# Kernel tuning notes

Measured on AMD Instinct MI355X. Metric: run time of the kernel, lower is better.

## Reference

```python
import jax, jax.numpy as jnp
import numpy as np

B, S, D = 1, 4096, 1024
H, Dh = 16, 64
F = 4096  # mlp_factor * D
EPS = 1e-6


def _ln(x, scale, bias=None):
    m = jnp.mean(x, axis=-1, keepdims=True)
    v = jnp.var(x, axis=-1, keepdims=True)
    y = (x - m) * jax.lax.rsqrt(v + EPS) * scale
    return y + bias if bias is not None else y


def setup_inputs() -> dict:
    key = jax.random.key(0)
    ks = jax.random.split(key, 10)
    lecun = lambda k, shape, fan_in: (jax.random.normal(k, shape, jnp.float32) * (fan_in ** -0.5))
    inp = {
        "x": jax.random.normal(ks[0], (B, S, D), jnp.float32),
        # causal mask, broadcastable to [B, H, S, S]
        "mask": jnp.tril(jnp.ones((S, S), bool))[None, None],
        # PreNorm (TPNorm -> LayerNorm)
        "ln_scale": jnp.ones((D,), jnp.float32),
        "ln_bias": jnp.zeros((D,), jnp.float32),
        # MLP input projection
        "w_in": lecun(ks[1], (D, F), D),
        "b_in": jnp.zeros((F,), jnp.float32),
        # QKV projection
        "wq": lecun(ks[2], (D, H, Dh), D),
        "bq": jnp.zeros((H, Dh), jnp.float32),
        "wk": lecun(ks[3], (D, H, Dh), D),
        "bk": jnp.zeros((H, Dh), jnp.float32),
        "wv": lecun(ks[4], (D, H, Dh), D),
        "bv": jnp.zeros((H, Dh), jnp.float32),
        # qk-norm scales (normalize_qk=True)
        "qn_scale": jnp.ones((Dh,), jnp.float32),
        "kn_scale": jnp.ones((Dh,), jnp.float32),
        # MLP output projection
        "w_mo": lecun(ks[5], (F, D), F),
        "b_mo": jnp.zeros((D,), jnp.float32),
        # Attention output projection
        "w_ao": lecun(ks[6], (H * Dh, D), H * Dh),
        "b_ao": jnp.zeros((D,), jnp.float32),
    }
    return inp


def reference(x, mask, ln_scale, ln_bias, w_in, b_in, wq, bq, wk, bk, wv, bv,
              qn_scale, kn_scale, w_mo, b_mo, w_ao, b_ao):
    residual = x
    xn = _ln(x, ln_scale, ln_bias)

    # fused QKV + MLP-input projections (QKVMLPDenseParallel)
    h = jax.nn.gelu(jnp.einsum("bsd,df->bsf", xn, w_in) + b_in)  # [B,S,F]
    q = jnp.einsum("bsd,dhk->bshk", xn, wq) + bq  # [B,S,H,Dh]
    k = jnp.einsum("bsd,dhk->bshk", xn, wk) + bk
    v = jnp.einsum("bsd,dhk->bshk", xn, wv) + bv
    # normalize_qk: per-head LayerNorm (no bias) on q, k
    q = _ln(q, qn_scale)
    k = _ln(k, kn_scale)

    # dot-product attention
    scores = jnp.einsum("bqhd,bkhd->bhqk", q, k) / np.sqrt(Dh).astype(np.float32)
    scores = jnp.where(mask, scores, jnp.finfo(scores.dtype).min)
    attn = jax.nn.softmax(scores, axis=-1)
    o = jnp.einsum("bhqk,bkhd->bqhd", attn, v)  # [B,S,H,Dh]

    # fused attention-out + MLP-out projections (AttnMLPOutParallel)
    mlp_out = jnp.einsum("bsf,fd->bsd", h, w_mo) + b_mo
    attn_out = jnp.einsum("bse,ed->bsd", o.reshape(B, S, H * Dh), w_ao) + b_ao

    # dropout deterministic (train=False); residual add
    return residual + mlp_out + attn_out
```

## Files before the change

kernel.cpp:

```cpp
#include <hip/hip_runtime.h>
#include <hip/hip_fp16.h>

typedef _Float16 half8 __attribute__((ext_vector_type(8)));
typedef float floatx4 __attribute__((ext_vector_type(4)));

constexpr int kS = 4096;
constexpr int kD = 1024;
constexpr int kH = 16;
constexpr int kDh = 64;
constexpr int kF = 4096;
constexpr int kNQKV = kF + 3 * kD;
constexpr int kKOut = kF + kD;

__device__ __forceinline__ void async_ld16(const void* g, void* l) {
  __builtin_amdgcn_global_load_lds(
      (const __attribute__((address_space(1))) void*)g,
      (__attribute__((address_space(3))) void*)l, 16, 0, 0);
}

__global__ __launch_bounds__(256) void prep0_kernel(
    const float* __restrict__ w_in, const float* __restrict__ wq,
    const float* __restrict__ wk, const float* __restrict__ wv,
    const float* __restrict__ w_mo, const float* __restrict__ w_ao,
    _Float16* __restrict__ Wqkv, _Float16* __restrict__ Wout,
    const float* __restrict__ x, const float* __restrict__ ln_scale,
    const float* __restrict__ ln_bias, _Float16* __restrict__ xn) {
  __shared__ float t[32][33];
  __shared__ float red[8];
  int id = blockIdx.x;
  const int tid = threadIdx.x;

  if (id >= 12288) {
    const int row = id - 12288;
    const float* xr = x + (size_t)row * kD;
    float v[4];
    float s = 0.f, sq = 0.f;
#pragma unroll
    for (int i = 0; i < 4; ++i) {
      v[i] = xr[tid + 256 * i];
      s += v[i];
      sq += v[i] * v[i];
    }
    for (int off = 32; off; off >>= 1) {
      s += __shfl_xor(s, off);
      sq += __shfl_xor(sq, off);
    }
    const int wv2 = tid >> 6;
    if ((tid & 63) == 0) { red[wv2] = s; red[wv2 + 4] = sq; }
    __syncthreads();
    s = red[0] + red[1] + red[2] + red[3];
    sq = red[4] + red[5] + red[6] + red[7];
    const float mean = s * (1.0f / kD);
    const float var = sq * (1.0f / kD) - mean * mean;
    const float rstd = rsqrtf(var + 1e-6f);
#pragma unroll
    for (int i = 0; i < 4; ++i) {
      int d = tid + 256 * i;
      xn[(size_t)row * kD + d] = (_Float16)((v[i] - mean) * rstd * ln_scale[d] + ln_bias[d]);
    }
    return;
  }

  const float* src; _Float16* dst; int N, ldk, noff, koff, nt, kt;
  if (id < 4096)       { src = w_in; dst = Wqkv; N = kF; ldk = kD; noff = 0;        koff = 0;  nt = id & 127; kt = id >> 7; }
  else if (id < 5120)  { id -= 4096; src = wq;  dst = Wqkv; N = kD; ldk = kD; noff = kF;       koff = 0;  nt = id & 31; kt = id >> 5; }
  else if (id < 6144)  { id -= 5120; src = wk;  dst = Wqkv; N = kD; ldk = kD; noff = kF + kD;  koff = 0;  nt = id & 31; kt = id >> 5; }
  else if (id < 7168)  { id -= 6144; src = wv;  dst = Wqkv; N = kD; ldk = kD; noff = kF + 2*kD; koff = 0; nt = id & 31; kt = id >> 5; }
  else if (id < 11264) { id -= 7168; src = w_mo; dst = Wout; N = kD; ldk = kKOut; noff = 0;    koff = 0;  nt = id & 31; kt = id >> 5; }
  else                 { id -= 11264; src = w_ao; dst = Wout; N = kD; ldk = kKOut; noff = 0;   koff = kF; nt = id & 31; kt = id >> 5; }
  const int n0 = nt * 32, k0 = kt * 32;
#pragma unroll
  for (int i = 0; i < 4; ++i) {
    const int kl = (tid >> 5) + i * 8, nl = tid & 31;
    t[kl][nl] = src[(size_t)(k0 + kl) * N + n0 + nl];
  }
  __syncthreads();
#pragma unroll
  for (int i = 0; i < 4; ++i) {
    const int nl = (tid >> 5) + i * 8, kl = tid & 31;
    dst[(size_t)(noff + n0 + nl) * ldk + koff + k0 + kl] = (_Float16)t[kl][nl];
  }
}

__global__ __launch_bounds__(256) void htrans_kernel(
    const _Float16* __restrict__ src, _Float16* __restrict__ dst, int R, int C) {
  __shared__ _Float16 t[32][34];
  const int tid = threadIdx.x;
  const int c0 = blockIdx.x * 32, r0 = blockIdx.y * 32;
#pragma unroll
  for (int i = 0; i < 4; ++i) {
    const int rl = (tid >> 5) + i * 8, cl = tid & 31;
    t[rl][cl] = src[(size_t)(r0 + rl) * C + c0 + cl];
  }
  __syncthreads();
#pragma unroll
  for (int i = 0; i < 4; ++i) {
    const int cl = (tid >> 5) + i * 8, rl = tid & 31;
    dst[(size_t)(c0 + cl) * R + r0 + rl] = t[rl][cl];
  }
}

__device__ __forceinline__ float fast_gelu(float xv) {
  const float z = 0.7978845608028654f * (xv + 0.044715f * xv * xv * xv);
  const float u = exp2f(fminf(2.885390081777927f * z, 80.0f));
  return xv * u / (1.0f + u);
}

__global__ __launch_bounds__(256) void gemm_qkvin(
    const _Float16* __restrict__ A, const _Float16* __restrict__ Bp,
    const float* __restrict__ b_in, const float* __restrict__ bq,
    const float* __restrict__ bk, const float* __restrict__ bv,
    const float* __restrict__ qn_scale, const float* __restrict__ kn_scale,
    _Float16* __restrict__ ho, _Float16* __restrict__ q,
    _Float16* __restrict__ k, _Float16* __restrict__ v) {
  __shared__ alignas(16) _Float16 Ts[2][16 * 512];

  const int tid = threadIdx.x;
  const int lane = tid & 63;
  const int wave = tid >> 6;
  const int wm = (wave >> 1) * 64;
  const int wn = (wave & 1) * 64;
  const int m0 = blockIdx.x * 128;
  const int n0 = blockIdx.y * 128;
  const int lrow = lane & 15;
  const int quad = lane >> 4;

  floatx4 acc[4][4] = {};

  auto stage = [&](int buf, int k0) {
#pragma unroll
    for (int i = 0; i < 4; ++i) {
      const int chunk = wave * 4 + i;
      const int r = ((chunk & 7) << 4) + (lane >> 2);
      const int csrc = ((lane & 3) ^ ((r >> 1) & 3)) << 3;
      const _Float16* src = (chunk < 8)
          ? A + (size_t)(m0 + r) * kD + k0 + csrc
          : Bp + (size_t)(n0 + r) * kD + k0 + csrc;
      async_ld16(src, &Ts[buf][chunk * 512]);
    }
  };

  stage(0, 0);
  asm volatile("s_waitcnt vmcnt(0)" ::: "memory");
  __builtin_amdgcn_s_barrier();

  int cur = 0;
  for (int k0 = 0; k0 < kD; k0 += 32) {
    if (k0 + 32 < kD) stage(cur ^ 1, k0 + 32);

    const _Float16* As = Ts[cur];
    const _Float16* Bs = Ts[cur] + 8 * 512;
    half8 af[4], bf[4];
#pragma unroll
    for (int i = 0; i < 4; ++i) {
      const int ra = wm + i * 16 + lrow;
      const int rb = wn + i * 16 + lrow;
      af[i] = *reinterpret_cast<const half8*>(&As[ra * 32 + ((quad ^ ((ra >> 1) & 3)) << 3)]);
      bf[i] = *reinterpret_cast<const half8*>(&Bs[rb * 32 + ((quad ^ ((rb >> 1) & 3)) << 3)]);
    }
#pragma unroll
    for (int i = 0; i < 4; ++i)
#pragma unroll
      for (int j = 0; j < 4; ++j)
        acc[i][j] = __builtin_amdgcn_mfma_f32_16x16x32_f16(af[i], bf[j], acc[i][j], 0, 0, 0);

    asm volatile("s_waitcnt vmcnt(0)" ::: "memory");
    __builtin_amdgcn_s_barrier();
    cur ^= 1;
  }

  const int nblk = n0 + wn;
  if (nblk < kF) {
#pragma unroll
    for (int i = 0; i < 4; ++i) {
      const int gm = m0 + wm + i * 16 + quad * 4;
#pragma unroll
      for (int j = 0; j < 4; ++j) {
        const int gn = nblk + j * 16 + lrow;
        const float bn = b_in[gn];
#pragma unroll
        for (int r = 0; r < 4; ++r)
          ho[(size_t)(gm + r) * kKOut + gn] = (_Float16)fast_gelu(acc[i][j][r] + bn);
      }
    }
  } else if (nblk >= kF + 2 * kD) {
#pragma unroll
    for (int i = 0; i < 4; ++i) {
      const int gm = m0 + wm + i * 16 + quad * 4;
#pragma unroll
      for (int j = 0; j < 4; ++j) {
        const int gn = nblk + j * 16 + lrow;
        const float bn = bv[(gn - kF) & (kD - 1)];
#pragma unroll
        for (int r = 0; r < 4; ++r)
          v[(size_t)(gm + r) * kD + ((gn - kF) & (kD - 1))] = (_Float16)(acc[i][j][r] + bn);
      }
    }
  } else {
    const bool isq = nblk < kF + kD;
    const float* nsc = isq ? qn_scale : kn_scale;
    const float* nb = isq ? bq : bk;
    const float sm = isq ? 0.18033688f : 1.0f;
    _Float16* dst = isq ? q : k;
    const int col0 = (nblk - kF) & (kD - 1);
    float bj[4];
#pragma unroll
    for (int j = 0; j < 4; ++j) bj[j] = nb[col0 + j * 16 + lrow];
#pragma unroll
    for (int i = 0; i < 4; ++i) {
      const int gm = m0 + wm + i * 16 + quad * 4;
#pragma unroll
      for (int r = 0; r < 4; ++r) {
        float vals[4], s1 = 0.f, s2 = 0.f;
#pragma unroll
        for (int j = 0; j < 4; ++j) {
          const float vv = acc[i][j][r] + bj[j];
          vals[j] = vv; s1 += vv; s2 += vv * vv;
        }
#pragma unroll
        for (int off = 1; off <= 8; off <<= 1) {
          s1 += __shfl_xor(s1, off);
          s2 += __shfl_xor(s2, off);
        }
        const float mean = s1 * (1.0f / 64.0f);
        const float rstd = rsqrtf(s2 * (1.0f / 64.0f) - mean * mean + 1e-6f);
#pragma unroll
        for (int j = 0; j < 4; ++j) {
          const int d = j * 16 + lrow;
          dst[(size_t)(gm + r) * kD + col0 + d] =
              (_Float16)((vals[j] - mean) * rstd * nsc[d] * sm);
        }
      }
    }
  }
}

__global__ __launch_bounds__(256) void prep_kernel(
    const float* __restrict__ x, const float* __restrict__ b_mo,
    const float* __restrict__ b_ao, float* __restrict__ out,
    float* __restrict__ Oacc, float* __restrict__ Lacc) {
  const int i = blockIdx.x * 256 + threadIdx.x;
  if (i < kS * kD) {
    const int d = i & (kD - 1);
    out[i] = x[i] + b_mo[d] + b_ao[d];
    Oacc[i] = 0.f;
  } else if (i < kS * kD + kS * kH) {
    Lacc[i - kS * kD] = 0.f;
  }
}

__global__ __launch_bounds__(256) void gemm_out(
    const _Float16* __restrict__ A, const _Float16* __restrict__ Bp,
    float* __restrict__ out) {
  __shared__ alignas(16) _Float16 Ts[2][16 * 512];

  const int tid = threadIdx.x;
  const int lane = tid & 63;
  const int wave = tid >> 6;
  const int wm = (wave >> 1) * 64;
  const int wn = (wave & 1) * 64;
  const int m0 = blockIdx.x * 128;
  const int n0 = blockIdx.y * 128;
  const int kbeg = blockIdx.z * (kKOut / 2);
  const int kend = kbeg + kKOut / 2;
  const int lrow = lane & 15;
  const int quad = lane >> 4;

  floatx4 acc[4][4] = {};

  auto stage = [&](int buf, int k0) {
#pragma unroll
    for (int i = 0; i < 4; ++i) {
      const int chunk = wave * 4 + i;
      const int r = ((chunk & 7) << 4) + (lane >> 2);
      const int csrc = ((lane & 3) ^ ((r >> 1) & 3)) << 3;
      const _Float16* src = (chunk < 8)
          ? A + (size_t)(m0 + r) * kKOut + k0 + csrc
          : Bp + (size_t)(n0 + r) * kKOut + k0 + csrc;
      async_ld16(src, &Ts[buf][chunk * 512]);
    }
  };

  stage(0, kbeg);
  asm volatile("s_waitcnt vmcnt(0)" ::: "memory");
  __builtin_amdgcn_s_barrier();

  int cur = 0;
  for (int k0 = kbeg; k0 < kend; k0 += 32) {
    if (k0 + 32 < kend) stage(cur ^ 1, k0 + 32);

    const _Float16* As = Ts[cur];
    const _Float16* Bs = Ts[cur] + 8 * 512;
    half8 af[4], bf[4];
#pragma unroll
    for (int i = 0; i < 4; ++i) {
      const int ra = wm + i * 16 + lrow;
      const int rb = wn + i * 16 + lrow;
      af[i] = *reinterpret_cast<const half8*>(&As[ra * 32 + ((quad ^ ((ra >> 1) & 3)) << 3)]);
      bf[i] = *reinterpret_cast<const half8*>(&Bs[rb * 32 + ((quad ^ ((rb >> 1) & 3)) << 3)]);
    }
#pragma unroll
    for (int i = 0; i < 4; ++i)
#pragma unroll
      for (int j = 0; j < 4; ++j)
        acc[i][j] = __builtin_amdgcn_mfma_f32_16x16x32_f16(af[i], bf[j], acc[i][j], 0, 0, 0);

    asm volatile("s_waitcnt vmcnt(0)" ::: "memory");
    __builtin_amdgcn_s_barrier();
    cur ^= 1;
  }

#pragma unroll
  for (int i = 0; i < 4; ++i) {
    const int gm = m0 + wm + i * 16 + quad * 4;
#pragma unroll
    for (int j = 0; j < 4; ++j) {
      const int gn = n0 + wn + j * 16 + lrow;
#pragma unroll
      for (int r = 0; r < 4; ++r)
        atomicAdd(out + (size_t)(gm + r) * kD + gn, acc[i][j][r]);
    }
  }
}

__global__ __launch_bounds__(256) void fattn_kernel(
    const _Float16* __restrict__ Q, const _Float16* __restrict__ K,
    const _Float16* __restrict__ Vt, float* __restrict__ Oacc,
    float* __restrict__ Lacc) {
  __shared__ alignas(16) _Float16 Qs[64 * 64];
  __shared__ alignas(16) _Float16 Ks[64 * 64];
  __shared__ alignas(16) _Float16 Vs[64 * 64];
  __shared__ alignas(16) _Float16 Ps[64 * 72];

  const int tid = threadIdx.x;
  const int lane = tid & 63;
  const int wave = tid >> 6;
  const int lrow = lane & 15;
  const int quad = lane >> 4;
  const int h = blockIdx.y;
  const int pair = blockIdx.x;
  const int split = blockIdx.z;

  const int rs = lane >> 3;
  const int cs = lane & 7;
  constexpr float kOff = 11.5415603f;

  for (int pass = 0; pass < 2; ++pass) {
    const int qtile = pass ? (63 - pair) : pair;
    const int qbase = qtile * 64;

    __syncthreads();
#pragma unroll
    for (int i = 0; i < 2; ++i) {
      const int chunk = wave * 2 + i;
      const int r = chunk * 8 + rs;
      async_ld16(Q + (size_t)(qbase + r) * kD + h * kDh + ((cs ^ (r & 7)) << 3),
                 Qs + chunk * 512);
    }
    __syncthreads();

    half8 qf[2];
#pragma unroll
    for (int kt = 0; kt < 2; ++kt) {
      const int row = wave * 16 + lrow;
      qf[kt] = *reinterpret_cast<const half8*>(
          &Qs[row * 64 + (((kt * 4 + quad) ^ (row & 7)) << 3)]);
    }

    float lst[4] = {0.f, 0.f, 0.f, 0.f};
    floatx4 oacc[4] = {};
    const int qw = qbase + wave * 16;

    for (int t = split; t <= qtile; t += 2) {
      const int k0 = t * 64;
      __syncthreads();
#pragma unroll
      for (int i = 0; i < 4; ++i) {
        const int c2 = wave * 4 + i;
        if (c2 < 8) {
          const int r = c2 * 8 + rs;
          async_ld16(K + (size_t)(k0 + r) * kD + h * kDh + ((cs ^ (r & 7)) << 3),
                     Ks + c2 * 512);
        } else {
          const int c = c2 - 8;
          const int r = c * 8 + rs;
          async_ld16(Vt + (size_t)(h * kDh + r) * kS + k0 + ((cs ^ (r & 7)) << 3),
                     Vs + c * 512);
        }
      }
      __syncthreads();

      const bool diag = (t == qtile);

      floatx4 sacc[4] = {};
#pragma unroll
      for (int jt = 0; jt < 4; ++jt) {
        if (diag && jt > wave) continue;
#pragma unroll
        for (int kt = 0; kt < 2; ++kt) {
          const int rb = jt * 16 + lrow;
          half8 bfk = *reinterpret_cast<const half8*>(
              &Ks[rb * 64 + (((kt * 4 + quad) ^ (rb & 7)) << 3)]);
          sacc[jt] = __builtin_amdgcn_mfma_f32_16x16x32_f16(qf[kt], bfk, sacc[jt], 0, 0, 0);
        }
      }

      if (diag) {
#pragma unroll
        for (int jt = 0; jt < 4; ++jt) {
          const int kg = k0 + jt * 16 + lrow;
#pragma unroll
          for (int r = 0; r < 4; ++r)
            if (kg > qw + quad * 4 + r) sacc[jt][r] = -1e30f;
        }
      }

#pragma unroll
      for (int jt = 0; jt < 4; ++jt)
#pragma unroll
        for (int r = 0; r < 4; ++r) {
          const float p = exp2f(sacc[jt][r] - kOff);
          sacc[jt][r] = p;
          lst[r] += p;
        }

#pragma unroll
      for (int jt = 0; jt < 4; ++jt)
#pragma unroll
        for (int r = 0; r < 4; ++r)
          Ps[(wave * 16 + quad * 4 + r) * 72 + jt * 16 + lrow] = (_Float16)sacc[jt][r];

      const int ktmax = (diag && wave < 2) ? 1 : 2;
      for (int kt = 0; kt < ktmax; ++kt) {
        half8 pf = *reinterpret_cast<const half8*>(
            &Ps[(wave * 16 + lrow) * 72 + (kt * 4 + quad) * 8]);
#pragma unroll
        for (int jt = 0; jt < 4; ++jt) {
          const int rb = jt * 16 + lrow;
          half8 vf = *reinterpret_cast<const half8*>(
              &Vs[rb * 64 + (((kt * 4 + quad) ^ (rb & 7)) << 3)]);
          oacc[jt] = __builtin_amdgcn_mfma_f32_16x16x32_f16(pf, vf, oacc[jt], 0, 0, 0);
        }
      }
    }

#pragma unroll
    for (int r = 0; r < 4; ++r)
#pragma unroll
      for (int off = 8; off; off >>= 1) lst[r] += __shfl_xor(lst[r], off);
#pragma unroll
    for (int r = 0; r < 4; ++r) {
      const int qg = qw + quad * 4 + r;
      if (lrow == 0) atomicAdd(Lacc + qg * kH + h, lst[r]);
#pragma unroll
      for (int jt = 0; jt < 4; ++jt)
        atomicAdd(Oacc + ((size_t)qg * kH + h) * kDh + jt * 16 + lrow, oacc[jt][r]);
    }
  }
}

__global__ __launch_bounds__(256) void norm_kernel(
    const float* __restrict__ Oacc, const float* __restrict__ Lacc,
    _Float16* __restrict__ ho) {
  const int idx = blockIdx.x * 256 + threadIdx.x;
  const int q = idx >> 10, rem = idx & 1023;
  const float l = Lacc[(q << 4) + (rem >> 6)];
  ho[(size_t)q * kKOut + kF + rem] = (_Float16)(Oacc[idx] / l);
}

extern "C" void kernel_launch(void* const* d_in, const int* in_sizes, int n_in,
                              void* d_out, int out_size, void* d_ws, size_t ws_size,
                              hipStream_t stream) {
  const float* x        = (const float*)d_in[0];
  const float* ln_scale = (const float*)d_in[2];
  const float* ln_bias  = (const float*)d_in[3];
  const float* w_in     = (const float*)d_in[4];
  const float* b_in     = (const float*)d_in[5];
  const float* wq       = (const float*)d_in[6];
  const float* bq       = (const float*)d_in[7];
  const float* wk       = (const float*)d_in[8];
  const float* bk       = (const float*)d_in[9];
  const float* wv       = (const float*)d_in[10];
  const float* bv       = (const float*)d_in[11];
  const float* qn_scale = (const float*)d_in[12];
  const float* kn_scale = (const float*)d_in[13];
  const float* w_mo     = (const float*)d_in[14];
  const float* b_mo     = (const float*)d_in[15];
  const float* w_ao     = (const float*)d_in[16];
  const float* b_ao     = (const float*)d_in[17];
  float* out = (float*)d_out;

  char* ws = (char*)d_ws;
  size_t off = 0;
  auto alloc = [&](size_t bytes) { char* p = ws + off; off += bytes; return p; };
  char* zone = (char*)alloc((size_t)kS * kD * 2 + (size_t)kNQKV * kD * 2);
  _Float16* xn   = (_Float16*)zone;
  _Float16* Wqkv = (_Float16*)(zone + (size_t)kS * kD * 2);
  float* Oacc = (float*)zone;
  float* Lacc = (float*)(zone + (size_t)kS * kD * 4);
  _Float16* Wout = (_Float16*)alloc((size_t)kD * kKOut * 2);
  _Float16* ho   = (_Float16*)alloc((size_t)kS * kKOut * 2);
  _Float16* q_h  = (_Float16*)alloc((size_t)kS * kD * 2);
  _Float16* k_h  = (_Float16*)alloc((size_t)kS * kD * 2);
  _Float16* v_h  = (_Float16*)alloc((size_t)kS * kD * 2);
  _Float16* v_t  = (_Float16*)alloc((size_t)kS * kD * 2);

  prep0_kernel<<<12288 + 4096, 256, 0, stream>>>(
      w_in, wq, wk, wv, w_mo, w_ao, Wqkv, Wout, x, ln_scale, ln_bias, xn);

  gemm_qkvin<<<dim3(kS / 128, kNQKV / 128), 256, 0, stream>>>(
      xn, Wqkv, b_in, bq, bk, bv, qn_scale, kn_scale, ho, q_h, k_h, v_h);

  htrans_kernel<<<dim3(kD / 32, kS / 32), 256, 0, stream>>>(v_h, v_t, kS, kD);

  prep_kernel<<<(kS * kD + kS * kH + 255) / 256, 256, 0, stream>>>(
      x, b_mo, b_ao, out, Oacc, Lacc);

  fattn_kernel<<<dim3(32, kH, 2), 256, 0, stream>>>(q_h, k_h, v_t, Oacc, Lacc);

  norm_kernel<<<kS * kD / 256, 256, 0, stream>>>(Oacc, Lacc, ho);

  gemm_out<<<dim3(kS / 128, kD / 128, 2), 256, 0, stream>>>(ho, Wout, out);
}
```

Before: 451.5 us.

## Enlarge QKV/MLP-in GEMM to 256x256 tiles with 8 waves and interleaved prefetch

Rewrites the fused input-projection GEMM to use 256x256 block tiles, 512 threads (8 waves, each computing 128x64), a BK=64 double-buffered LDS pipeline split into quarter stages interleaved with MFMA groups, s_setprio around MFMA bursts, and an XCD-aware block-id remap. The aim is to raise arithmetic intensity per LDS/global load and overlap memory with compute better. In exchange it uses 128KB of LDS and many more accumulator registers, which may limit occupancy, and adds many barriers.

```diff
diff --git a/kernel.cpp b/kernel.cpp
--- a/kernel.cpp
+++ b/kernel.cpp
@@ -17,6 +17,8 @@
       (const __attribute__((address_space(1))) void*)g,
       (__attribute__((address_space(3))) void*)l, 16, 0, 0);
 }
+
+#define CFENCE() asm volatile("" ::: "memory")
 
 __global__ __launch_bounds__(256) void prep0_kernel(
     const float* __restrict__ w_in, const float* __restrict__ wq,
@@ -106,116 +108,167 @@
   return xv * u / (1.0f + u);
 }
 
-__global__ __launch_bounds__(256) void gemm_qkvin(
+__global__ __launch_bounds__(512, 2) void gemm_qkvin(
     const _Float16* __restrict__ A, const _Float16* __restrict__ Bp,
     const float* __restrict__ b_in, const float* __restrict__ bq,
     const float* __restrict__ bk, const float* __restrict__ bv,
     const float* __restrict__ qn_scale, const float* __restrict__ kn_scale,
     _Float16* __restrict__ ho, _Float16* __restrict__ q,
     _Float16* __restrict__ k, _Float16* __restrict__ v) {
-  __shared__ alignas(16) _Float16 Ts[2][16 * 512];
+  __shared__ alignas(16) _Float16 Ts[65536];
 
   const int tid = threadIdx.x;
   const int lane = tid & 63;
   const int wave = tid >> 6;
-  const int wm = (wave >> 1) * 64;
-  const int wn = (wave & 1) * 64;
-  const int m0 = blockIdx.x * 128;
-  const int n0 = blockIdx.y * 128;
+  const int wr = wave >> 2;
+  const int wc = wave & 3;
   const int lrow = lane & 15;
   const int quad = lane >> 4;
 
-  floatx4 acc[4][4] = {};
-
-  auto stage = [&](int buf, int k0) {
-#pragma unroll
-    for (int i = 0; i < 4; ++i) {
-      const int chunk = wave * 4 + i;
-      const int r = ((chunk & 7) << 4) + (lane >> 2);
-      const int csrc = ((lane & 3) ^ ((r >> 1) & 3)) << 3;
-      const _Float16* src = (chunk < 8)
-          ? A + (size_t)(m0 + r) * kD + k0 + csrc
-          : Bp + (size_t)(n0 + r) * kD + k0 + csrc;
-      async_ld16(src, &Ts[buf][chunk * 512]);
-    }
+  int bid = blockIdx.y * 16 + blockIdx.x;
+  bid = (bid & 7) * 56 + (bid >> 3);
+  const int m0 = (bid & 15) * 256;
+  const int n0 = (bid >> 4) * 256;
+
+  const int swz = ((quad ^ (lrow & 3)) << 3);
+  const int aoff = (wr * 128 + lrow) * 32 + swz;
+  const int boff = 16384 + (wc * 64 + lrow) * 32 + swz;
+
+  const int srow = wave * 32 + (lane >> 2);
+  const int scol = (((lane & 3) ^ ((lane >> 2) & 3)) << 3);
+  const int sldsl = wave * 1024;
+
+  floatx4 acc[8][4] = {};
+
+  auto stage = [&](int nb, int p, int kb) {
+    const int mat = p & 1;
+    const int lds0 = nb * 32768 + mat * 16384 + (p >> 1) * 8192 + sldsl;
+    const _Float16* g0 = (mat == 0)
+        ? A + (size_t)(m0 + srow) * kD + kb + scol
+        : Bp + (size_t)(n0 + srow) * kD + kb + scol;
+    async_ld16(g0, Ts + lds0);
+    async_ld16(g0 + (size_t)16 * kD, Ts + lds0 + 512);
   };
 
-  stage(0, 0);
-  asm volatile("s_waitcnt vmcnt(0)" ::: "memory");
-  __builtin_amdgcn_s_barrier();
-
-  int cur = 0;
-  for (int k0 = 0; k0 < kD; k0 += 32) {
-    if (k0 + 32 < kD) stage(cur ^ 1, k0 + 32);
-
-    const _Float16* As = Ts[cur];
-    const _Float16* Bs = Ts[cur] + 8 * 512;
-    half8 af[4], bf[4];
-#pragma unroll
-    for (int i = 0; i < 4; ++i) {
-      const int ra = wm + i * 16 + lrow;
-      const int rb = wn + i * 16 + lrow;
-      af[i] = *reinterpret_cast<const half8*>(&As[ra * 32 + ((quad ^ ((ra >> 1) & 3)) << 3)]);
-      bf[i] = *reinterpret_cast<const half8*>(&Bs[rb * 32 + ((quad ^ ((rb >> 1) & 3)) << 3)]);
-    }
-#pragma unroll
-    for (int i = 0; i < 4; ++i)
-#pragma unroll
-      for (int j = 0; j < 4; ++j)
-        acc[i][j] = __builtin_amdgcn_mfma_f32_16x16x32_f16(af[i], bf[j], acc[i][j], 0, 0, 0);
-
-    asm volatile("s_waitcnt vmcnt(0)" ::: "memory");
-    __builtin_amdgcn_s_barrier();
-    cur ^= 1;
-  }
-
-  const int nblk = n0 + wn;
-  if (nblk < kF) {
-#pragma unroll
-    for (int i = 0; i < 4; ++i) {
-      const int gm = m0 + wm + i * 16 + quad * 4;
-#pragma unroll
-      for (int j = 0; j < 4; ++j) {
-        const int gn = nblk + j * 16 + lrow;
+  stage(0, 0, 0);
+  stage(0, 1, 0);
+  stage(0, 2, 32);
+  stage(0, 3, 32);
+  asm volatile("s_waitcnt vmcnt(4)" ::: "memory");
+  CFENCE(); __builtin_amdgcn_s_barrier(); CFENCE();
+
+  half8 af[8];
+  constexpr int NT = kD / 64;
+  for (int t = 0; t < NT; ++t) {
+    const int cur = t & 1, nb = cur ^ 1;
+    const int co = cur * 32768;
+    const bool pf = (t + 1 < NT);
+    const int kb1 = (t + 1) * 64;
+
+    auto rdA = [&](int ks) {
+#pragma unroll
+      for (int mi = 0; mi < 8; ++mi)
+        af[mi] = *reinterpret_cast<const half8*>(Ts + co + ks * 8192 + aoff + mi * 512);
+    };
+    auto rdB = [&](int ks, int nf) -> half8 {
+      return *reinterpret_cast<const half8*>(Ts + co + ks * 8192 + boff + nf * 512);
+    };
+    half8 bf0, bf1;
+
+    auto mm2 = [&](int nf0, half8 b0, half8 b1) {
+      __builtin_amdgcn_s_setprio(1);
+#pragma unroll
+      for (int mi = 0; mi < 8; ++mi)
+        acc[mi][nf0] = __builtin_amdgcn_mfma_f32_16x16x32_f16(af[mi], b0, acc[mi][nf0], 0, 0, 0);
+#pragma unroll
+      for (int mi = 0; mi < 8; ++mi)
+        acc[mi][nf0 + 1] = __builtin_amdgcn_mfma_f32_16x16x32_f16(af[mi], b1, acc[mi][nf0 + 1], 0, 0, 0);
+      __builtin_amdgcn_s_setprio(0);
+    };
+
+    rdA(0); bf0 = rdB(0, 0); bf1 = rdB(0, 1);
+    if (pf) stage(nb, 0, kb1);
+    CFENCE(); __builtin_amdgcn_s_barrier(); CFENCE();
+    mm2(0, bf0, bf1);
+    CFENCE(); __builtin_amdgcn_s_barrier(); CFENCE();
+
+    bf0 = rdB(0, 2); bf1 = rdB(0, 3);
+    if (pf) {
+      stage(nb, 1, kb1);
+      asm volatile("s_waitcnt vmcnt(4)" ::: "memory");
+    } else {
+      asm volatile("s_waitcnt vmcnt(0)" ::: "memory");
+    }
+    CFENCE(); __builtin_amdgcn_s_barrier(); CFENCE();
+    mm2(2, bf0, bf1);
+    CFENCE(); __builtin_amdgcn_s_barrier(); CFENCE();
+
+    rdA(1); bf0 = rdB(1, 0); bf1 = rdB(1, 1);
+    if (pf) stage(nb, 2, kb1 + 32);
+    CFENCE(); __builtin_amdgcn_s_barrier(); CFENCE();
+    mm2(0, bf0, bf1);
+    CFENCE(); __builtin_amdgcn_s_barrier(); CFENCE();
+
+    bf0 = rdB(1, 2); bf1 = rdB(1, 3);
+    if (pf) {
+      stage(nb, 3, kb1 + 32);
+      asm volatile("s_waitcnt vmcnt(4)" ::: "memory");
+    }
+    CFENCE(); __builtin_amdgcn_s_barrier(); CFENCE();
+    mm2(2, bf0, bf1);
+    CFENCE(); __builtin_amdgcn_s_barrier(); CFENCE();
+  }
+
+  const int nblk0 = n0 + wc * 64;
+  const int rbase = m0 + wr * 128 + quad * 4;
+
+  if (nblk0 < kF) {
+#pragma unroll
+    for (int mi = 0; mi < 8; ++mi) {
+      const int gm = rbase + mi * 16;
+#pragma unroll
+      for (int nf = 0; nf < 4; ++nf) {
+        const int gn = nblk0 + nf * 16 + lrow;
         const float bn = b_in[gn];
 #pragma unroll
         for (int r = 0; r < 4; ++r)
-          ho[(size_t)(gm + r) * kKOut + gn] = (_Float16)fast_gelu(acc[i][j][r] + bn);
-      }
-    }
-  } else if (nblk >= kF + 2 * kD) {
-#pragma unroll
-    for (int i = 0; i < 4; ++i) {
-      const int gm = m0 + wm + i * 16 + quad * 4;
-#pragma unroll
-      for (int j = 0; j < 4; ++j) {
-        const int gn = nblk + j * 16 + lrow;
-        const float bn = bv[(gn - kF) & (kD - 1)];
+          ho[(size_t)(gm + r) * kKOut + gn] = (_Float16)fast_gelu(acc[mi][nf][r] + bn);
+      }
+    }
+  } else if (nblk0 >= kF + 2 * kD) {
+    const int cb = nblk0 - (kF + 2 * kD);
+#pragma unroll
+    for (int mi = 0; mi < 8; ++mi) {
+      const int gm = rbase + mi * 16;
+#pragma unroll
+      for (int nf = 0; nf < 4; ++nf) {
+        const int col = cb + nf * 16 + lrow;
+        const float bn = bv[col];
 #pragma unroll
         for (int r = 0; r < 4; ++r)
-          v[(size_t)(gm + r) * kD + ((gn - kF) & (kD - 1))] = (_Float16)(acc[i][j][r] + bn);
+          v[(size_t)(gm + r) * kD + col] = (_Float16)(acc[mi][nf][r] + bn);
       }
     }
   } else {
-    const bool isq = nblk < kF + kD;
+    const bool isq = nblk0 < kF + kD;
     const float* nsc = isq ? qn_scale : kn_scale;
-    const float* nb = isq ? bq : bk;
+    const float* nb2 = isq ? bq : bk;
     const float sm = isq ? 0.18033688f : 1.0f;
     _Float16* dst = isq ? q : k;
-    const int col0 = (nblk - kF) & (kD - 1);
+    const int col0 = (nblk0 - kF) & (kD - 1);
     float bj[4];
 #pragma unroll
-    for (int j = 0; j < 4; ++j) bj[j] = nb[col0 + j * 16 + lrow];
-#pragma unroll
-    for (int i = 0; i < 4; ++i) {
-      const int gm = m0 + wm + i * 16 + quad * 4;
+    for (int nf = 0; nf < 4; ++nf) bj[nf] = nb2[col0 + nf * 16 + lrow];
+#pragma unroll
+    for (int mi = 0; mi < 8; ++mi) {
+      const int gm = rbase + mi * 16;
 #pragma unroll
       for (int r = 0; r < 4; ++r) {
         float vals[4], s1 = 0.f, s2 = 0.f;
 #pragma unroll
-        for (int j = 0; j < 4; ++j) {
-          const float vv = acc[i][j][r] + bj[j];
-          vals[j] = vv; s1 += vv; s2 += vv * vv;
+        for (int nf = 0; nf < 4; ++nf) {
+          const float vv = acc[mi][nf][r] + bj[nf];
+          vals[nf] = vv; s1 += vv; s2 += vv * vv;
         }
 #pragma unroll
         for (int off = 1; off <= 8; off <<= 1) {
@@ -225,10 +278,10 @@
         const float mean = s1 * (1.0f / 64.0f);
         const float rstd = rsqrtf(s2 * (1.0f / 64.0f) - mean * mean + 1e-6f);
 #pragma unroll
-        for (int j = 0; j < 4; ++j) {
-          const int d = j * 16 + lrow;
+        for (int nf = 0; nf < 4; ++nf) {
+          const int d = nf * 16 + lrow;
           dst[(size_t)(gm + r) * kD + col0 + d] =
-              (_Float16)((vals[j] - mean) * rstd * nsc[d] * sm);
+              (_Float16)((vals[nf] - mean) * rstd * nsc[d] * sm);
         }
       }
     }
@@ -508,7 +561,7 @@
   prep0_kernel<<<12288 + 4096, 256, 0, stream>>>(
       w_in, wq, wk, wv, w_mo, w_ao, Wqkv, Wout, x, ln_scale, ln_bias, xn);
 
-  gemm_qkvin<<<dim3(kS / 128, kNQKV / 128), 256, 0, stream>>>(
+  gemm_qkvin<<<dim3(kS / 256, kNQKV / 256), 512, 0, stream>>>(
       xn, Wqkv, b_in, bq, bk, bv, qn_scale, kn_scale, ho, q_h, k_h, v_h);
 
   htrans_kernel<<<dim3(kD / 32, kS / 32), 256, 0, stream>>>(v_h, v_t, kS, kD);
```

New measurement: 447.4 us (median of 2 runs). Within noise of the previous version (-0.9%).
